# Kernel optimization log

Hardware: AMD Instinct MI355X
Metric: run time of the kernel (lower is better)

Reference implementation:

```python
import jax, jax.numpy as jnp
import numpy as np

RES = (64, 64)
TEMP = 0.1  # forward default temp

def _mgrid(res):
    # matches torch.meshgrid(linspace(0, r-1, r)...) with default 'ij' indexing
    gs = jnp.meshgrid(*[jnp.arange(r, dtype=jnp.float32) for r in res], indexing='ij')
    return jnp.stack(gs, 0)  # [2, H, W]

def setup_inputs() -> dict:
    key = jax.random.key(0)
    k1, k2 = jax.random.split(key)
    x = jax.random.normal(k1, (8, 32, RES[0], RES[1]), dtype=jnp.float32)
    of = jax.random.normal(k2, (8, 2, RES[0], RES[1]), dtype=jnp.float32)
    return {"x": x, "of": of}

def reference(x, of):
    bs, C = x.shape[0], x.shape[1]
    hw = RES[0] * RES[1]
    gpos = _mgrid(RES).reshape(2, hw)                 # [2, HW] target pixel positions
    opos = gpos[None] + of.reshape(bs, 2, hw)         # [bs, 2, HW] flow-displaced source positions
    # L1 distance: logits[b, i, j] = sum_c |opos[b, c, j] - gpos[c, i]|
    dist = jnp.abs(opos[:, :, None, :] - gpos[None, :, :, None]).sum(axis=1)  # [bs, HW, HW]
    # softmax over target axis i (dim=-2 in torch) -> each source pixel j distributes mass over targets
    locs = jax.nn.softmax(-dist / TEMP, axis=1)       # [bs, HW, HW]
    # out[b, c, i] = sum_j x[b, c, j] * locs[b, i, j]
    out = jnp.einsum('bij,bcj->bci', locs, x.reshape(bs, C, hw))
    return out.reshape(bs, C, RES[0], RES[1])
```

## Files before the change

kernel.cpp:

```cpp
#include <hip/hip_runtime.h>
#include <hip/hip_fp16.h>
#include <math.h>

#define HW    4096
#define NC    32
#define NB    8
#define TINV  10.0f
#define RWIN  8
#define WDIM  (8 + 2 * RWIN)
#define RCUT  1.2f
#define MAXS  148


__device__ __forceinline__ __half2 u32_as_h2(unsigned int u) {
    union { unsigned int u; __half2 h; } c; c.u = u; return c.h;
}
__device__ __forceinline__ unsigned int h2_as_u32(__half2 h) {
    union { __half2 h; unsigned int u; } c; c.h = h; return c.u;
}

__global__ __launch_bounds__(256) void prep_kernel(
    const float* __restrict__ x, const float* __restrict__ of,
    float4* __restrict__ params, unsigned int* __restrict__ xt2u)
{
    __shared__ float tile[32][66];
    const int bx = blockIdx.x;
    const int b  = bx >> 6;
    const int j0 = (bx & 63) << 6;
    const int t  = threadIdx.x;
    const int jj = t & 63;
    const int wN = t >> 6;

    if (t < 64) {
        int j = j0 + t;
        float oy = (float)(j >> 6) + of[(b * 2 + 0) * HW + j];
        float ox = (float)(j & 63) + of[(b * 2 + 1) * HW + j];
        int cy0 = min(max((int)floorf(oy), 0), 63);
        int cx0 = min(max((int)floorf(ox), 0), 63);
        float Dy = 0.f, Dx = 0.f;
        #pragma unroll
        for (int d = -3; d <= 3; ++d) {
            int iy = cy0 + d, ix = cx0 + d;
            if ((unsigned)iy < 64u) Dy += __expf(-TINV * fabsf(oy - (float)iy));
            if ((unsigned)ix < 64u) Dx += __expf(-TINV * fabsf(ox - (float)ix));
        }
        params[(b << 12) + j] = make_float4(oy, ox, 1.f / Dy, 1.f / Dx);
    }

    #pragma unroll
    for (int k = 0; k < 8; ++k) {
        int c = wN * 8 + k;
        tile[c][jj] = x[((size_t)(b * NC + c) << 12) + j0 + jj];
    }
    __syncthreads();

    {
        int j2 = t >> 2, q = t & 3;
        int c0 = q << 3;
        uint4 o;
        o.x = h2_as_u32(__floats2half2_rn(tile[c0 + 0][j2], tile[c0 + 1][j2]));
        o.y = h2_as_u32(__floats2half2_rn(tile[c0 + 2][j2], tile[c0 + 3][j2]));
        o.z = h2_as_u32(__floats2half2_rn(tile[c0 + 4][j2], tile[c0 + 5][j2]));
        o.w = h2_as_u32(__floats2half2_rn(tile[c0 + 6][j2], tile[c0 + 7][j2]));
        *(uint4*)&xt2u[((size_t)((b << 12) + j0 + j2) << 4) + (q << 2)] = o;
    }
}

__global__ __launch_bounds__(256) void gather_kernel(
    const float4* __restrict__ params, const unsigned int* __restrict__ xtu,
    float* __restrict__ out)
{
    __shared__ __align__(16) unsigned int pool[4 * MAXS * 4 + 4 * MAXS + 4096];

    const int b    = blockIdx.y;
    const int tile = blockIdx.x;
    const int ty0  = (tile >> 3) << 3;
    const int tx0  = (tile & 7) << 3;

    const int tid  = threadIdx.x;
    const int lane = tid & 63;
    const int wv   = __builtin_amdgcn_readfirstlane(tid >> 6);

    float4*       wpW = ((float4*)pool) + wv * MAXS;
    int*          sjW = ((int*)pool) + 4 * MAXS * 4 + wv * MAXS;
    unsigned int* XSW = pool + 4 * MAXS * 4 + 4 * MAXS + wv * 1024;

    const float iy = (float)(ty0 + (lane >> 3));
    const float ix = (float)(tx0 + (lane & 7));

    __half2 acc16[16];
    #pragma unroll
    for (int c = 0; c < 16; ++c) acc16[c] = __floats2half2_rn(0.f, 0.f);

    const float4*       pb = params + (b << 12);
    const unsigned int* xb = xtu + ((size_t)(b << 12) << 4);

    const int srow = lane >> 5;
    const int scol = lane & 31;

    float4 pr3[3]; int jr3[3]; bool va3[3];
    #pragma unroll
    for (int r = 0; r < 3; ++r) {
        int ry = wv + srow * 4 + r * 8;
        int jy = ty0 - RWIN + ry;
        int jx = tx0 - RWIN + scol;
        bool valid = ((unsigned)jy < 64u) && ((unsigned)jx < 64u) && (scol < WDIM);
        int j = (jy << 6) + jx;
        va3[r] = valid; jr3[r] = j;
        pr3[r] = pb[valid ? j : 0];
    }

    int total = 0;
    #pragma unroll
    for (int r = 0; r < 3; ++r) {
        float4 p = pr3[r];
        float cy = fminf(fmaxf(p.x, 0.f), 63.f);
        float cx = fminf(fmaxf(p.y, 0.f), 63.f);
        float dyr = fmaxf(fmaxf((float)ty0 - cy, cy - ((float)ty0 + 7.f)), 0.f);
        float dxr = fmaxf(fmaxf((float)tx0 - cx, cx - ((float)tx0 + 7.f)), 0.f);
        bool pred = va3[r] && (dyr + dxr < RCUT);
        unsigned long long m = __ballot(pred);
        if (pred) {
            int pos = total + __builtin_amdgcn_mbcnt_hi((unsigned)(m >> 32),
                              __builtin_amdgcn_mbcnt_lo((unsigned)m, 0u));
            wpW[pos] = p;
            sjW[pos] = jr3[r];
        }
        total += __popcll(m);
    }
    if ((total & 1) && lane == 0) {
        wpW[total] = make_float4(1.f, 1.f, 0.f, 0.f);
        sjW[total] = sjW[0];
    }
    const int padT = total + (total & 1);
    const int nch  = (padT + 31) >> 5;

    auto stage_load = [&](int c, uint4& A, uint4& B) {
        int s = (c << 5) + (lane >> 1);
        A = make_uint4(0u, 0u, 0u, 0u); B = A;
        if (s < padT) {
            const unsigned int* src = xb + (size_t)sjW[s] * 16 + ((lane & 1) << 3);
            A = *(const uint4*)src;
            B = *(const uint4*)(src + 4);
        }
    };
    auto stage_write = [&](int c, uint4 A, uint4 B) {
        unsigned int* d = XSW + ((c & 1) << 9) + (lane << 3);
        *(uint4*)d       = A;
        *(uint4*)(d + 4) = B;
    };

    if (nch > 0) {
        uint4 a0, b0;
        stage_load(0, a0, b0);
        stage_write(0, a0, b0);
        for (int c = 0; c < nch; ++c) {
            uint4 na, nb;
            const bool more = (c + 1) < nch;
            if (more) stage_load(c + 1, na, nb);

            int cnt_c = min(32, padT - (c << 5));
            const uint4* XR = (const uint4*)(XSW + ((c & 1) << 9));
            for (int k = 0; k < cnt_c; k += 2) {
                float4 p0 = wpW[(c << 5) + k], p1 = wpW[(c << 5) + k + 1];
                const uint4* x0 = XR + (k << 2);
                const uint4* x1 = XR + ((k + 1) << 2);
                uint4 A[4], Bv[4];
                #pragma unroll
                for (int q = 0; q < 4; ++q) { A[q] = x0[q]; Bv[q] = x1[q]; }

                float g0 = (__expf(-TINV * fabsf(p0.x - iy)) * p0.z)
                         * (__expf(-TINV * fabsf(p0.y - ix)) * p0.w);
                float g1 = (__expf(-TINV * fabsf(p1.x - iy)) * p1.z)
                         * (__expf(-TINV * fabsf(p1.y - ix)) * p1.w);
                __half2 hg0 = __float2half2_rn(g0);
                __half2 hg1 = __float2half2_rn(g1);

                #pragma unroll
                for (int q = 0; q < 4; ++q) {
                    acc16[4 * q + 0] = __hfma2(hg0, u32_as_h2(A[q].x), acc16[4 * q + 0]);
                    acc16[4 * q + 1] = __hfma2(hg0, u32_as_h2(A[q].y), acc16[4 * q + 1]);
                    acc16[4 * q + 2] = __hfma2(hg0, u32_as_h2(A[q].z), acc16[4 * q + 2]);
                    acc16[4 * q + 3] = __hfma2(hg0, u32_as_h2(A[q].w), acc16[4 * q + 3]);
                }
                #pragma unroll
                for (int q = 0; q < 4; ++q) {
                    acc16[4 * q + 0] = __hfma2(hg1, u32_as_h2(Bv[q].x), acc16[4 * q + 0]);
                    acc16[4 * q + 1] = __hfma2(hg1, u32_as_h2(Bv[q].y), acc16[4 * q + 1]);
                    acc16[4 * q + 2] = __hfma2(hg1, u32_as_h2(Bv[q].z), acc16[4 * q + 2]);
                    acc16[4 * q + 3] = __hfma2(hg1, u32_as_h2(Bv[q].w), acc16[4 * q + 3]);
                }
            }
            if (more) stage_write(c + 1, na, nb);
        }
    }

    __syncthreads();
    unsigned int* redu = pool;
    unsigned int* myr  = redu + (unsigned)tid * 17;
    #pragma unroll
    for (int c = 0; c < 16; ++c) myr[c] = h2_as_u32(acc16[c]);
    __syncthreads();

    int t  = tid & 63;
    int c0 = tid >> 6;
    #pragma unroll
    for (int k = 0; k < 4; ++k) {
        int c2 = c0 + (k << 2);
        float sx = 0.f, sy = 0.f;
        #pragma unroll
        for (int w = 0; w < 4; ++w) {
            float2 f = __half22float2(u32_as_h2(redu[(unsigned)((w << 6) + t) * 17 + c2]));
            sx += f.x; sy += f.y;
        }
        int ch   = c2 << 1;
        int base = (((b << 5) + ch) << 12) + (ty0 + (t >> 3)) * 64 + (tx0 + (t & 7));
        out[base]      = sx;
        out[base + HW] = sy;
    }
}

extern "C" void kernel_launch(void* const* d_in, const int* in_sizes, int n_in,
                              void* d_out, int out_size, void* d_ws, size_t ws_size,
                              hipStream_t stream) {
    const float* x  = (const float*)d_in[0];
    const float* of = (const float*)d_in[1];
    float* out = (float*)d_out;

    float4*       params = (float4*)d_ws;
    unsigned int* xt2u   = (unsigned int*)((char*)d_ws + NB * HW * sizeof(float4));

    prep_kernel<<<dim3(NB * 64), dim3(256), 0, stream>>>(x, of, params, xt2u);
    gather_kernel<<<dim3(64, NB), dim3(256), 0, stream>>>(
        params, xt2u, out);
}
```

Measured before the change: 65.51 us.

## Split gather window rows across eight waves and stage all sources at once

The gather kernel now launches 512 threads (8 waves) per tile instead of 256. Each wave scans 3 window rows instead of 6, so per-wave candidate lists shrink (MAXS drops from 148 to 76). Each wave loads all its candidate x vectors into LDS up front rather than double-buffering in 32-entry chunks, and the final reduction sums across 8 waves. This shortens each wave's serial accumulation loop and adds parallelism across the 512 blocks, at the cost of more LDS per block, a larger cross-wave reduction, and no overlap between global loads and compute.

```diff
diff --git a/kernel.cpp b/kernel.cpp
--- a/kernel.cpp
+++ b/kernel.cpp
@@ -9,7 +9,7 @@
 #define RWIN  8
 #define WDIM  (8 + 2 * RWIN)
 #define RCUT  1.2f
-#define MAXS  148
+#define MAXS  76
 
 
 __device__ __forceinline__ __half2 u32_as_h2(unsigned int u) {
@@ -66,11 +66,11 @@
     }
 }
 
-__global__ __launch_bounds__(256) void gather_kernel(
+__global__ __launch_bounds__(512, 4) void gather_kernel(
     const float4* __restrict__ params, const unsigned int* __restrict__ xtu,
     float* __restrict__ out)
 {
-    __shared__ __align__(16) unsigned int pool[4 * MAXS * 4 + 4 * MAXS + 4096];
+    __shared__ __align__(16) unsigned int pool[12768];
 
     const int b    = blockIdx.y;
     const int tile = blockIdx.x;
@@ -82,8 +82,8 @@
     const int wv   = __builtin_amdgcn_readfirstlane(tid >> 6);
 
     float4*       wpW = ((float4*)pool) + wv * MAXS;
-    int*          sjW = ((int*)pool) + 4 * MAXS * 4 + wv * MAXS;
-    unsigned int* XSW = pool + 4 * MAXS * 4 + 4 * MAXS + wv * 1024;
+    int*          sjW = ((int*)pool) + 8 * MAXS * 4 + wv * MAXS;
+    unsigned int* XSW = pool + 8 * MAXS * 4 + 8 * MAXS + wv * (MAXS * 16);
 
     const float iy = (float)(ty0 + (lane >> 3));
     const float ix = (float)(tx0 + (lane & 7));
@@ -95,16 +95,13 @@
     const float4*       pb = params + (b << 12);
     const unsigned int* xb = xtu + ((size_t)(b << 12) << 4);
 
-    const int srow = lane >> 5;
-    const int scol = lane & 31;
-
     float4 pr3[3]; int jr3[3]; bool va3[3];
     #pragma unroll
     for (int r = 0; r < 3; ++r) {
-        int ry = wv + srow * 4 + r * 8;
+        int ry = wv + (r << 3);
         int jy = ty0 - RWIN + ry;
-        int jx = tx0 - RWIN + scol;
-        bool valid = ((unsigned)jy < 64u) && ((unsigned)jx < 64u) && (scol < WDIM);
+        int jx = tx0 - RWIN + lane;
+        bool valid = ((unsigned)jy < 64u) && ((unsigned)jx < 64u) && (lane < WDIM);
         int j = (jy << 6) + jx;
         va3[r] = valid; jr3[r] = j;
         pr3[r] = pb[valid ? j : 0];
@@ -133,65 +130,47 @@
         sjW[total] = sjW[0];
     }
     const int padT = total + (total & 1);
-    const int nch  = (padT + 31) >> 5;
-
-    auto stage_load = [&](int c, uint4& A, uint4& B) {
-        int s = (c << 5) + (lane >> 1);
-        A = make_uint4(0u, 0u, 0u, 0u); B = A;
+
+    for (int m0 = 0; m0 < padT; m0 += 32) {
+        int s = m0 + (lane >> 1);
         if (s < padT) {
             const unsigned int* src = xb + (size_t)sjW[s] * 16 + ((lane & 1) << 3);
-            A = *(const uint4*)src;
-            B = *(const uint4*)(src + 4);
-        }
-    };
-    auto stage_write = [&](int c, uint4 A, uint4 B) {
-        unsigned int* d = XSW + ((c & 1) << 9) + (lane << 3);
-        *(uint4*)d       = A;
-        *(uint4*)(d + 4) = B;
-    };
-
-    if (nch > 0) {
-        uint4 a0, b0;
-        stage_load(0, a0, b0);
-        stage_write(0, a0, b0);
-        for (int c = 0; c < nch; ++c) {
-            uint4 na, nb;
-            const bool more = (c + 1) < nch;
-            if (more) stage_load(c + 1, na, nb);
-
-            int cnt_c = min(32, padT - (c << 5));
-            const uint4* XR = (const uint4*)(XSW + ((c & 1) << 9));
-            for (int k = 0; k < cnt_c; k += 2) {
-                float4 p0 = wpW[(c << 5) + k], p1 = wpW[(c << 5) + k + 1];
-                const uint4* x0 = XR + (k << 2);
-                const uint4* x1 = XR + ((k + 1) << 2);
-                uint4 A[4], Bv[4];
-                #pragma unroll
-                for (int q = 0; q < 4; ++q) { A[q] = x0[q]; Bv[q] = x1[q]; }
-
-                float g0 = (__expf(-TINV * fabsf(p0.x - iy)) * p0.z)
-                         * (__expf(-TINV * fabsf(p0.y - ix)) * p0.w);
-                float g1 = (__expf(-TINV * fabsf(p1.x - iy)) * p1.z)
-                         * (__expf(-TINV * fabsf(p1.y - ix)) * p1.w);
-                __half2 hg0 = __float2half2_rn(g0);
-                __half2 hg1 = __float2half2_rn(g1);
-
-                #pragma unroll
-                for (int q = 0; q < 4; ++q) {
-                    acc16[4 * q + 0] = __hfma2(hg0, u32_as_h2(A[q].x), acc16[4 * q + 0]);
-                    acc16[4 * q + 1] = __hfma2(hg0, u32_as_h2(A[q].y), acc16[4 * q + 1]);
-                    acc16[4 * q + 2] = __hfma2(hg0, u32_as_h2(A[q].z), acc16[4 * q + 2]);
-                    acc16[4 * q + 3] = __hfma2(hg0, u32_as_h2(A[q].w), acc16[4 * q + 3]);
-                }
-                #pragma unroll
-                for (int q = 0; q < 4; ++q) {
-                    acc16[4 * q + 0] = __hfma2(hg1, u32_as_h2(Bv[q].x), acc16[4 * q + 0]);
-                    acc16[4 * q + 1] = __hfma2(hg1, u32_as_h2(Bv[q].y), acc16[4 * q + 1]);
-                    acc16[4 * q + 2] = __hfma2(hg1, u32_as_h2(Bv[q].z), acc16[4 * q + 2]);
-                    acc16[4 * q + 3] = __hfma2(hg1, u32_as_h2(Bv[q].w), acc16[4 * q + 3]);
-                }
-            }
-            if (more) stage_write(c + 1, na, nb);
+            uint4 A = *(const uint4*)src;
+            uint4 B = *(const uint4*)(src + 4);
+            unsigned int* d = XSW + (s << 4) + ((lane & 1) << 3);
+            *(uint4*)d       = A;
+            *(uint4*)(d + 4) = B;
+        }
+    }
+
+    for (int k = 0; k < padT; k += 2) {
+        float4 p0 = wpW[k], p1 = wpW[k + 1];
+        const uint4* x0 = (const uint4*)(XSW + (k << 4));
+        const uint4* x1 = (const uint4*)(XSW + ((k + 1) << 4));
+        uint4 A[4], Bv[4];
+        #pragma unroll
+        for (int q = 0; q < 4; ++q) { A[q] = x0[q]; Bv[q] = x1[q]; }
+
+        float g0 = (__expf(-TINV * fabsf(p0.x - iy)) * p0.z)
+                 * (__expf(-TINV * fabsf(p0.y - ix)) * p0.w);
+        float g1 = (__expf(-TINV * fabsf(p1.x - iy)) * p1.z)
+                 * (__expf(-TINV * fabsf(p1.y - ix)) * p1.w);
+        __half2 hg0 = __float2half2_rn(g0);
+        __half2 hg1 = __float2half2_rn(g1);
+
+        #pragma unroll
+        for (int q = 0; q < 4; ++q) {
+            acc16[4 * q + 0] = __hfma2(hg0, u32_as_h2(A[q].x), acc16[4 * q + 0]);
+            acc16[4 * q + 1] = __hfma2(hg0, u32_as_h2(A[q].y), acc16[4 * q + 1]);
+            acc16[4 * q + 2] = __hfma2(hg0, u32_as_h2(A[q].z), acc16[4 * q + 2]);
+            acc16[4 * q + 3] = __hfma2(hg0, u32_as_h2(A[q].w), acc16[4 * q + 3]);
+        }
+        #pragma unroll
+        for (int q = 0; q < 4; ++q) {
+            acc16[4 * q + 0] = __hfma2(hg1, u32_as_h2(Bv[q].x), acc16[4 * q + 0]);
+            acc16[4 * q + 1] = __hfma2(hg1, u32_as_h2(Bv[q].y), acc16[4 * q + 1]);
+            acc16[4 * q + 2] = __hfma2(hg1, u32_as_h2(Bv[q].z), acc16[4 * q + 2]);
+            acc16[4 * q + 3] = __hfma2(hg1, u32_as_h2(Bv[q].w), acc16[4 * q + 3]);
         }
     }
 
@@ -205,11 +184,11 @@
     int t  = tid & 63;
     int c0 = tid >> 6;
     #pragma unroll
-    for (int k = 0; k < 4; ++k) {
-        int c2 = c0 + (k << 2);
+    for (int k = 0; k < 2; ++k) {
+        int c2 = c0 + (k << 3);
         float sx = 0.f, sy = 0.f;
         #pragma unroll
-        for (int w = 0; w < 4; ++w) {
+        for (int w = 0; w < 8; ++w) {
             float2 f = __half22float2(u32_as_h2(redu[(unsigned)((w << 6) + t) * 17 + c2]));
             sx += f.x; sy += f.y;
         }
@@ -231,6 +210,6 @@
     unsigned int* xt2u   = (unsigned int*)((char*)d_ws + NB * HW * sizeof(float4));
 
     prep_kernel<<<dim3(NB * 64), dim3(256), 0, stream>>>(x, of, params, xt2u);
-    gather_kernel<<<dim3(64, NB), dim3(256), 0, stream>>>(
+    gather_kernel<<<dim3(64, NB), dim3(512), 0, stream>>>(
         params, xt2u, out);
 }
```

Result: no change. 65.34 us (-0.3%).
